# Kernel tuning notes

Hardware: AMD Instinct MI355X
Metric: run time of the kernel (lower is better)

Reference implementation:

```python
import jax, jax.numpy as jnp
import numpy as np

B, NB, D, H = 16384, 3, 1024, 8
HD = D // H
EPS = 1e-5

def setup_inputs() -> dict:
    key = jax.random.key(0)
    ks = jax.random.split(key, 24)
    w = lambda k, shp: jax.random.normal(k, shp, jnp.float32) * 0.02
    return {
        "x": jax.random.normal(ks[0], (B, NB, D), jnp.float32),
        # nn.MultiheadAttention params
        "in_proj_w": w(ks[1], (3 * D, D)),
        "in_proj_b": jnp.zeros((3 * D,), jnp.float32),
        "out_w": w(ks[2], (D, D)),
        "out_b": jnp.zeros((D,), jnp.float32),
        # weight_generator MLP
        "wg1_w": w(ks[3], (D, D * NB)), "wg1_b": jnp.zeros((D,), jnp.float32),
        "wg2_w": w(ks[4], (D // 2, D)), "wg2_b": jnp.zeros((D // 2,), jnp.float32),
        "wg3_w": w(ks[5], (NB, D // 2)), "wg3_b": jnp.zeros((NB,), jnp.float32),
        # refiner MLP + LayerNorms
        "r1_w": w(ks[6], (2 * D, D)), "r1_b": jnp.zeros((2 * D,), jnp.float32),
        "ln1_g": jnp.ones((2 * D,), jnp.float32), "ln1_b": jnp.zeros((2 * D,), jnp.float32),
        "r2_w": w(ks[7], (D, 2 * D)), "r2_b": jnp.zeros((D,), jnp.float32),
        "ln2_g": jnp.ones((D,), jnp.float32), "ln2_b": jnp.zeros((D,), jnp.float32),
    }

def _layernorm(x, g, b):
    m = jnp.mean(x, axis=-1, keepdims=True)
    v = jnp.mean(jnp.square(x - m), axis=-1, keepdims=True)
    return (x - m) * jax.lax.rsqrt(v + EPS) * g + b

def _forward(x, in_proj_w, in_proj_b, out_w, out_b,
             wg1_w, wg1_b, wg2_w, wg2_b, wg3_w, wg3_b,
             r1_w, r1_b, ln1_g, ln1_b, r2_w, r2_b, ln2_g, ln2_b):
    b = x.shape[0]
    # --- cross (self) attention over the NB branch tokens ---
    qkv = jnp.einsum("bsd,ed->bse", x, in_proj_w) + in_proj_b  # [B, NB, 3D]
    q, k, v = jnp.split(qkv, 3, axis=-1)
    q = q.reshape(b, NB, H, HD)
    k = k.reshape(b, NB, H, HD)
    v = v.reshape(b, NB, H, HD)
    scores = jnp.einsum("bqhd,bkhd->bhqk", q, k) / jnp.sqrt(jnp.float32(HD))
    attn = jax.nn.softmax(scores, axis=-1)
    o = jnp.einsum("bhqk,bkhd->bqhd", attn, v).reshape(b, NB, D)
    attended = jnp.einsum("bsd,ed->bse", o, out_w) + out_b  # [B, NB, D]
    # --- dynamic softmax gate over branches ---
    flat = attended.reshape(b, NB * D)
    h = jax.nn.relu(flat @ wg1_w.T + wg1_b)
    h = jax.nn.relu(h @ wg2_w.T + wg2_b)
    weights = jax.nn.softmax(h @ wg3_w.T + wg3_b, axis=-1)  # [B, NB]
    weighted = jnp.einsum("bsd,bs->bd", attended, weights)  # [B, D]
    # --- refiner (dropout inactive in eval) ---
    h = weighted @ r1_w.T + r1_b
    h = jax.nn.relu(_layernorm(h, ln1_g, ln1_b))
    out = h @ r2_w.T + r2_b
    return _layernorm(out, ln2_g, ln2_b)

def reference(x, in_proj_w, in_proj_b, out_w, out_b,
              wg1_w, wg1_b, wg2_w, wg2_b, wg3_w, wg3_b,
              r1_w, r1_b, ln1_g, ln1_b, r2_w, r2_b, ln2_g, ln2_b):
    return _forward(x, in_proj_w, in_proj_b, out_w, out_b,
                    wg1_w, wg1_b, wg2_w, wg2_b, wg3_w, wg3_b,
                    r1_w, r1_b, ln1_g, ln1_b, r2_w, r2_b, ln2_g, ln2_b)
```

## Files before the change

### kernel.cpp

```cpp
#include <hip/hip_runtime.h>
#include <hip/hip_bf16.h>

#define BB   16384
#define NBR  3
#define DD   1024
#define HH   8
#define HDD  128

typedef __attribute__((ext_vector_type(8))) short short8;
typedef __attribute__((ext_vector_type(4))) float f32x4;

__device__ __forceinline__ float b2f(ushort u) {
    union { unsigned int i; float f; } x; x.i = ((unsigned int)u) << 16; return x.f;
}
__device__ __forceinline__ ushort f2b(float f) {
    union { __hip_bfloat16 h; ushort u; } x; x.h = __float2bfloat16(f); return x.u;
}

__global__ __launch_bounds__(256) void cvt_f32_bf16(const float* __restrict__ in,
                                                    ushort* __restrict__ out, long n) {
    long i = ((long)blockIdx.x * 256 + threadIdx.x) * 4;
    if (i + 4 > n) return;
    float4 v = *reinterpret_cast<const float4*>(in + i);
    unsigned int a = ((unsigned int)f2b(v.x)) | (((unsigned int)f2b(v.y)) << 16);
    unsigned int b = ((unsigned int)f2b(v.z)) | (((unsigned int)f2b(v.w)) << 16);
    uint2 p; p.x = a; p.y = b;
    *reinterpret_cast<uint2*>(out + i) = p;
}

__global__ __launch_bounds__(256) void transpose_cvt(const float* __restrict__ in,
                                                     ushort* __restrict__ out) {
    __shared__ float t[32][33];
    const int bx = blockIdx.x & 31, by = blockIdx.x >> 5;
    const int tx = threadIdx.x & 31, ty = threadIdx.x >> 5;
    #pragma unroll
    for (int i = 0; i < 4; i++)
        t[ty + i * 8][tx] = in[(size_t)(by * 32 + ty + i * 8) * 1024 + bx * 32 + tx];
    __syncthreads();
    #pragma unroll
    for (int i = 0; i < 4; i++)
        out[(size_t)(bx * 32 + ty + i * 8) * 1024 + by * 32 + tx] = f2b(t[tx][ty + i * 8]);
}

__global__ __launch_bounds__(256) void bias1_kernel(const float* __restrict__ wg1w,
                                                    const float* __restrict__ wg1b,
                                                    const float* __restrict__ outb,
                                                    float* __restrict__ b1p) {
    const int o = (blockIdx.x * 256 + threadIdx.x) >> 6;
    const int lane = threadIdx.x & 63;
    const float* wr = wg1w + (size_t)o * 3072;
    float s = 0.f;
    for (int e = lane; e < 1024; e += 64)
        s += outb[e] * (wr[e] + wr[e + 1024] + wr[e + 2048]);
    #pragma unroll
    for (int off = 32; off; off >>= 1) s += __shfl_xor(s, off, 64);
    if (lane == 0) b1p[o] = s + wg1b[o];
}

__global__ __launch_bounds__(256) void biasfold_kernel(const float* __restrict__ w,
                                                       const float* __restrict__ bin,
                                                       const float* __restrict__ badd,
                                                       float* __restrict__ outb, int K) {
    const int o = (blockIdx.x * 256 + threadIdx.x) >> 6;
    const int lane = threadIdx.x & 63;
    const float* wr = w + (size_t)o * K;
    float s = 0.f;
    for (int e = lane; e < K; e += 64) s += bin[e] * wr[e];
    #pragma unroll
    for (int off = 32; off; off >>= 1) s += __shfl_xor(s, off, 64);
    if (lane == 0) outb[o] = s + badd[o];
}

#define CPAD 258
template<int EPI>
__global__ __launch_bounds__(512, 2)
void gemm256(const ushort* __restrict__ A, const ushort* __restrict__ Bt,
             const float* __restrict__ bias, void* __restrict__ Cout,
             int M, int N, int K) {
    extern __shared__ ushort lds[];

    const int tid  = threadIdx.x;
    const int wid  = tid >> 6;
    const int lane = tid & 63;
    const int cpx  = gridDim.x >> 3;
    const int bid  = (blockIdx.x & 7) * cpx + (blockIdx.x >> 3);
    const int nbn  = N >> 8;
    const int bm   = bid / nbn;
    const int bn   = bid % nbn;
    const long m0  = (long)bm * 256;
    const long n0  = (long)bn * 256;
    const int NT   = K >> 6;

    const int srow = tid >> 3;
    const int kel  = (((tid & 7) ^ (srow & 7)) << 3);
    const int widEl = wid * 512;

    const ushort* gA[2][2];
    const ushort* gB[2][2];
    #pragma unroll
    for (int c = 0; c < 2; c++)
        #pragma unroll
        for (int j = 0; j < 2; j++) {
            gA[c][j] = A  + (size_t)(m0 + c * 128 + j * 64 + srow) * K + kel;
            gB[c][j] = Bt + (size_t)(n0 + c * 128 + j * 64 + srow) * K + kel;
        }

    const int wr = wid >> 2, wc = wid & 3;
    const int lm15 = lane & 15;
    int aoff[8];
    #pragma unroll
    for (int m = 0; m < 8; m++) aoff[m] = (wr * 128 + m * 16 + lm15) * 64;
    int boff[4];
    #pragma unroll
    for (int c = 0; c < 4; c++) boff[c] = (wc * 64 + c * 16 + lm15) * 64;
    const int kbr[2] = {
        (((0 << 6) | ((lane >> 4) << 4)) ^ ((lane & 7) << 4)) >> 1,
        (((1 << 6) | ((lane >> 4) << 4)) ^ ((lane & 7) << 4)) >> 1
    };

    f32x4 acc[8][4];
    #pragma unroll
    for (int m = 0; m < 8; m++)
        #pragma unroll
        for (int c = 0; c < 4; c++) { f32x4 z = {0.f, 0.f, 0.f, 0.f}; acc[m][c] = z; }

    short8 af[8], af2[8], bf[2], bf2[2];

#define STAGE(C, PB, TT) { \
    const ushort* _g0; const ushort* _g1; int _b; \
    if ((C) < 2) { _g0 = gA[(C)][0] + (TT) * 64; _g1 = gA[(C)][1] + (TT) * 64; \
                   _b = (PB) * 16384 + (C) * 8192 + widEl; } \
    else         { _g0 = gB[(C) - 2][0] + (TT) * 64; _g1 = gB[(C) - 2][1] + (TT) * 64; \
                   _b = 32768 + (PB) * 16384 + ((C) - 2) * 8192 + widEl; } \
    __builtin_amdgcn_global_load_lds((const __attribute__((address_space(1))) void*)_g0, \
        (__attribute__((address_space(3))) void*)&lds[_b], 16, 0, 0); \
    __builtin_amdgcn_global_load_lds((const __attribute__((address_space(1))) void*)_g1, \
        (__attribute__((address_space(3))) void*)&lds[_b + 4096], 16, 0, 0); }

#define READ_A(DST, P, KK) { \
    _Pragma("unroll") \
    for (int _m = 0; _m < 8; _m++) \
        DST[_m] = *(const short8*)&lds[(P) * 16384 + aoff[_m] + kbr[KK]]; }

#define READ_B2(DST, P, KK, C0) { \
    DST[0] = *(const short8*)&lds[32768 + (P) * 16384 + boff[(C0)] + kbr[KK]]; \
    DST[1] = *(const short8*)&lds[32768 + (P) * 16384 + boff[(C0) + 1] + kbr[KK]]; }

#define MFMA8x2(AF, BF, C0) { \
    _Pragma("unroll") \
    for (int _m = 0; _m < 8; _m++) { \
        acc[_m][(C0)]     = __builtin_amdgcn_mfma_f32_16x16x32_bf16(AF[_m], BF[0], acc[_m][(C0)], 0, 0, 0); \
        acc[_m][(C0) + 1] = __builtin_amdgcn_mfma_f32_16x16x32_bf16(AF[_m], BF[1], acc[_m][(C0) + 1], 0, 0, 0); } }

#define TILE_STEP(P, T, PRE) { \
     \
    if (PRE) STAGE(0, (P) ^ 1, (T) + 1); \
    if (PRE) { asm volatile("s_waitcnt vmcnt(2)" ::: "memory"); } \
    else     { asm volatile("s_waitcnt vmcnt(0)" ::: "memory"); } \
    __builtin_amdgcn_s_barrier(); \
    asm volatile("" ::: "memory"); \
    __builtin_amdgcn_sched_barrier(0); \
     \
    READ_A(af, P, 0); \
    READ_B2(bf, P, 0, 0); \
    __builtin_amdgcn_s_setprio(1); MFMA8x2(af, bf, 0); __builtin_amdgcn_s_setprio(0); \
    if (PRE) STAGE(1, (P) ^ 1, (T) + 1); \
    READ_B2(bf2, P, 0, 2); \
    __builtin_amdgcn_s_barrier(); \
     \
    __builtin_amdgcn_s_setprio(1); MFMA8x2(af, bf2, 2); __builtin_amdgcn_s_setprio(0); \
    if (PRE) STAGE(2, (P) ^ 1, (T) + 1); \
    READ_A(af2, P, 1); \
    READ_B2(bf, P, 1, 0); \
    __builtin_amdgcn_s_barrier(); \
     \
    __builtin_amdgcn_s_setprio(1); MFMA8x2(af2, bf, 0); __builtin_amdgcn_s_setprio(0); \
    if (PRE) STAGE(3, (P) ^ 1, (T) + 1); \
    READ_B2(bf2, P, 1, 2); \
    __builtin_amdgcn_s_barrier(); \
     \
    __builtin_amdgcn_s_setprio(1); MFMA8x2(af2, bf2, 2); __builtin_amdgcn_s_setprio(0); \
    __builtin_amdgcn_s_barrier(); }

    STAGE(0, 0, 0); STAGE(1, 0, 0); STAGE(2, 0, 0); STAGE(3, 0, 0);

    int t = 0;
    for (; t + 2 < NT; t += 2) {
        TILE_STEP(0, t, true);
        TILE_STEP(1, t + 1, true);
    }
    TILE_STEP(0, t, true);
    TILE_STEP(1, t + 1, false);

#undef TILE_STEP
#undef MFMA8x2
#undef READ_B2
#undef READ_A
#undef STAGE

    const int l16 = lane >> 4;
    #pragma unroll
    for (int c = 0; c < 4; c++) {
        const int colc = wc * 64 + c * 16 + lm15;
        const float bc = bias[n0 + colc];
        #pragma unroll
        for (int m = 0; m < 8; m++) {
            const int rowb = wr * 128 + m * 16 + l16 * 4;
            #pragma unroll
            for (int j = 0; j < 4; j++) {
                float v = acc[m][c][j] + bc;
                if (EPI == 1) v = v > 0.f ? v : 0.f;
                lds[(rowb + j) * CPAD + colc] = f2b(v);
            }
        }
    }
    __syncthreads();
    {
        const int r0 = tid >> 5;
        const int c0 = (tid & 31) * 8;
        #pragma unroll
        for (int it = 0; it < 16; it++) {
            const int row = it * 16 + r0;
            short8 val = *(const short8*)&lds[row * CPAD + c0];
            *reinterpret_cast<short8*>(&((ushort*)Cout)[(m0 + row) * (long)N + n0 + c0]) = val;
        }
    }
}

template<int EPI>
__global__ __launch_bounds__(256, 2)
void gemm_bt(const ushort* __restrict__ A, const ushort* __restrict__ Bt,
             const float* __restrict__ bias, void* __restrict__ Cout,
             int M, int N, int K, int lda, int ldb, int ldc, int sA, int sC) {
    __shared__ ushort As[128 * 64];
    __shared__ ushort Bs[128 * 64];
    const int tid  = threadIdx.x;
    const int wid  = tid >> 6;
    const int lane = tid & 63;
    const int cpx  = gridDim.x >> 3;
    const int bid  = (blockIdx.x & 7) * cpx + (blockIdx.x >> 3);
    const int nbn  = N >> 7;
    const int bm   = bid / nbn;
    const int bn   = bid % nbn;
    const long m0  = (long)bm * 128;
    const long n0  = (long)bn * 128;

    A += (size_t)blockIdx.y * sA;
    const long cOff = (long)blockIdx.y * sC;

    const int srow = tid >> 3;
    const int scol = (tid & 7) << 3;
    const ushort* gA = A  + (m0 + srow) * (long)lda + scol;
    const ushort* gB = Bt + (n0 + srow) * (long)ldb + scol;

    f32x4 acc[4][4];
    #pragma unroll
    for (int i = 0; i < 4; i++)
        #pragma unroll
        for (int j = 0; j < 4; j++) { f32x4 z = {0.f, 0.f, 0.f, 0.f}; acc[i][j] = z; }

    const int wr = wid >> 1, wc = wid & 1;
    const int kits = K >> 6;

    for (int kt = 0; kt < kits; ++kt) {
        const ushort* pA = gA + kt * 64;
        const ushort* pB = gB + kt * 64;
        #pragma unroll
        for (int i = 0; i < 4; i++) {
            __builtin_amdgcn_global_load_lds(
                (const __attribute__((address_space(1))) void*)(pA + (long)i * 32 * lda),
                (__attribute__((address_space(3))) void*)&As[(i * 32 + wid * 8) * 64],
                16, 0, 0);
        }
        #pragma unroll
        for (int i = 0; i < 4; i++) {
            __builtin_amdgcn_global_load_lds(
                (const __attribute__((address_space(1))) void*)(pB + (long)i * 32 * ldb),
                (__attribute__((address_space(3))) void*)&Bs[(i * 32 + wid * 8) * 64],
                16, 0, 0);
        }
        __syncthreads();
        #pragma unroll
        for (int kk = 0; kk < 2; kk++) {
            const int ko = kk * 32 + (lane >> 4) * 8;
            short8 af[4], bf[4];
            #pragma unroll
            for (int m = 0; m < 4; m++)
                af[m] = *(const short8*)&As[(wr * 64 + m * 16 + (lane & 15)) * 64 + ko];
            #pragma unroll
            for (int n = 0; n < 4; n++)
                bf[n] = *(const short8*)&Bs[(wc * 64 + n * 16 + (lane & 15)) * 64 + ko];
            #pragma unroll
            for (int m = 0; m < 4; m++)
                #pragma unroll
                for (int n = 0; n < 4; n++)
                    acc[m][n] = __builtin_amdgcn_mfma_f32_16x16x32_bf16(af[m], bf[n], acc[m][n], 0, 0, 0);
        }
        __syncthreads();
    }

    #pragma unroll
    for (int n = 0; n < 4; n++) {
        const long c = n0 + wc * 64 + n * 16 + (lane & 15);
        const float bc = bias[c];
        #pragma unroll
        for (int m = 0; m < 4; m++) {
            const long r = m0 + wr * 64 + m * 16 + (lane >> 4) * 4;
            #pragma unroll
            for (int j = 0; j < 4; j++) {
                float v = acc[m][n][j] + bc;
                if (EPI == 1) v = v > 0.f ? v : 0.f;
                ((ushort*)Cout)[(r + j) * (long)ldc + cOff + c] = f2b(v);
            }
        }
    }
}

__global__ __launch_bounds__(256) void attn_kernel(const ushort* __restrict__ qkv,
                                                   ushort* __restrict__ o) {
    const int w    = (blockIdx.x * 256 + threadIdx.x) >> 6;
    const int lane = threadIdx.x & 63;
    const int b = w >> 3, h = w & 7;
    const ushort* base = qkv + (size_t)b * (3 * 3072) + h * HDD + lane * 2;

    float q[3][2], k[3][2], v[3][2];
    #pragma unroll
    for (int i = 0; i < 3; i++) {
        unsigned int qu = *(const unsigned int*)(base + i * 3072);
        unsigned int ku = *(const unsigned int*)(base + i * 3072 + 1024);
        unsigned int vu = *(const unsigned int*)(base + i * 3072 + 2048);
        q[i][0] = b2f((ushort)(qu & 0xffff)); q[i][1] = b2f((ushort)(qu >> 16));
        k[i][0] = b2f((ushort)(ku & 0xffff)); k[i][1] = b2f((ushort)(ku >> 16));
        v[i][0] = b2f((ushort)(vu & 0xffff)); v[i][1] = b2f((ushort)(vu >> 16));
    }

    float s[3][3];
    #pragma unroll
    for (int i = 0; i < 3; i++)
        #pragma unroll
        for (int j = 0; j < 3; j++)
            s[i][j] = q[i][0] * k[j][0] + q[i][1] * k[j][1];

    #pragma unroll
    for (int off = 32; off; off >>= 1)
        #pragma unroll
        for (int i = 0; i < 3; i++)
            #pragma unroll
            for (int j = 0; j < 3; j++)
                s[i][j] += __shfl_xor(s[i][j], off, 64);

    const float sc = 0.08838834764831845f;
    float a[3][3];
    #pragma unroll
    for (int i = 0; i < 3; i++) {
        float l0 = s[i][0] * sc, l1 = s[i][1] * sc, l2 = s[i][2] * sc;
        float mx = fmaxf(fmaxf(l0, l1), l2);
        float e0 = __expf(l0 - mx), e1 = __expf(l1 - mx), e2 = __expf(l2 - mx);
        float inv = 1.f / (e0 + e1 + e2);
        a[i][0] = e0 * inv; a[i][1] = e1 * inv; a[i][2] = e2 * inv;
    }

    ushort* ob = o + (size_t)b * 3072 + h * HDD + lane * 2;
    #pragma unroll
    for (int i = 0; i < 3; i++) {
        float o0 = a[i][0] * v[0][0] + a[i][1] * v[1][0] + a[i][2] * v[2][0];
        float o1 = a[i][0] * v[0][1] + a[i][1] * v[1][1] + a[i][2] * v[2][1];
        unsigned int pk = ((unsigned int)f2b(o0)) | (((unsigned int)f2b(o1)) << 16);
        *(unsigned int*)(ob + i * 1024) = pk;
    }
}

__global__ __launch_bounds__(256) void gate_kernel(const ushort* __restrict__ h2,
                                                   const float* __restrict__ w3,
                                                   const float* __restrict__ b3,
                                                   const ushort* __restrict__ att,
                                                   ushort* __restrict__ weighted) {
    const int gw = (blockIdx.x * 256 + threadIdx.x) >> 6;
    const int lane = threadIdx.x & 63;
    if (gw >= BB) return;

    const ushort* hr = h2 + (size_t)gw * 512 + lane * 8;
    short8 hv = *(const short8*)hr;
    float hf[8];
    #pragma unroll
    for (int d = 0; d < 8; d++) hf[d] = b2f((ushort)hv[d]);

    float dot[3];
    #pragma unroll
    for (int s = 0; s < 3; s++) {
        const float* wr = w3 + s * 512 + lane * 8;
        float4 wa = *(const float4*)wr;
        float4 wb = *(const float4*)(wr + 4);
        dot[s] = hf[0] * wa.x + hf[1] * wa.y + hf[2] * wa.z + hf[3] * wa.w
               + hf[4] * wb.x + hf[5] * wb.y + hf[6] * wb.z + hf[7] * wb.w;
    }
    #pragma unroll
    for (int off = 32; off; off >>= 1)
        #pragma unroll
        for (int s = 0; s < 3; s++) dot[s] += __shfl_xor(dot[s], off, 64);

    float l0 = dot[0] + b3[0], l1 = dot[1] + b3[1], l2 = dot[2] + b3[2];
    float mx = fmaxf(fmaxf(l0, l1), l2);
    float e0 = __expf(l0 - mx), e1 = __expf(l1 - mx), e2 = __expf(l2 - mx);
    float inv = 1.f / (e0 + e1 + e2);
    float w0 = e0 * inv, w1 = e1 * inv, w2 = e2 * inv;

    const ushort* ab = att + (size_t)gw * 3072;
    ushort* wb = weighted + (size_t)gw * 1024;
    #pragma unroll
    for (int i = 0; i < 2; i++) {
        int d0 = (i * 64 + lane) * 8;
        short8 a0 = *(const short8*)(ab + d0);
        short8 a1 = *(const short8*)(ab + 1024 + d0);
        short8 a2 = *(const short8*)(ab + 2048 + d0);
        short8 r;
        #pragma unroll
        for (int d = 0; d < 8; d++) {
            float v = w0 * b2f((ushort)a0[d]) + w1 * b2f((ushort)a1[d]) + w2 * b2f((ushort)a2[d]);
            r[d] = (short)f2b(v);
        }
        *(short8*)(wb + d0) = r;
    }
}

template<int W, int RELU, int OUTBF16>
__global__ __launch_bounds__(256) void ln_kernel(const ushort* __restrict__ in,
                                                 const float* __restrict__ g,
                                                 const float* __restrict__ bt,
                                                 void* __restrict__ out) {
    constexpr int E = W / 256;
    const int row = blockIdx.x;
    const ushort* xr = in + (size_t)row * W + threadIdx.x * E;

    float v[E];
    if (E == 8) {
        uint4 raw = *reinterpret_cast<const uint4*>(xr);
        const unsigned int* rw = (const unsigned int*)&raw;
        #pragma unroll
        for (int p = 0; p < 4; p++) {
            v[2 * p]     = b2f((ushort)(rw[p] & 0xffff));
            v[2 * p + 1] = b2f((ushort)(rw[p] >> 16));
        }
    } else {
        uint2 raw = *reinterpret_cast<const uint2*>(xr);
        const unsigned int* rw = (const unsigned int*)&raw;
        #pragma unroll
        for (int p = 0; p < 2; p++) {
            v[2 * p]     = b2f((ushort)(rw[p] & 0xffff));
            v[2 * p + 1] = b2f((ushort)(rw[p] >> 16));
        }
    }

    float s = 0.f;
    #pragma unroll
    for (int e = 0; e < E; e++) s += v[e];

    __shared__ float red1[4], red2[4];
    const int wid = threadIdx.x >> 6, lane = threadIdx.x & 63;
    #pragma unroll
    for (int off = 32; off; off >>= 1) s += __shfl_xor(s, off, 64);
    if (lane == 0) red1[wid] = s;
    __syncthreads();
    const float mean = (red1[0] + red1[1] + red1[2] + red1[3]) / (float)W;

    float q = 0.f;
    #pragma unroll
    for (int e = 0; e < E; e++) { float d = v[e] - mean; q += d * d; }
    #pragma unroll
    for (int off = 32; off; off >>= 1) q += __shfl_xor(q, off, 64);
    if (lane == 0) red2[wid] = q;
    __syncthreads();
    const float var = (red2[0] + red2[1] + red2[2] + red2[3]) / (float)W;
    const float rstd = rsqrtf(var + 1e-5f);

    const int c0 = threadIdx.x * E;
    float o[E];
    #pragma unroll
    for (int e = 0; e < E; e++) {
        float ov = (v[e] - mean) * rstd * g[c0 + e] + bt[c0 + e];
        if (RELU) ov = ov > 0.f ? ov : 0.f;
        o[e] = ov;
    }
    if (OUTBF16) {
        ushort* op = (ushort*)out + (size_t)row * W + c0;
        unsigned int pk[E / 2];
        #pragma unroll
        for (int p = 0; p < E / 2; p++)
            pk[p] = ((unsigned int)f2b(o[2 * p])) | (((unsigned int)f2b(o[2 * p + 1])) << 16);
        if (E == 8) *reinterpret_cast<uint4*>(op) = *(uint4*)pk;
        else        *reinterpret_cast<uint2*>(op) = *(uint2*)pk;
    } else {
        float* op = (float*)out + (size_t)row * W + c0;
        #pragma unroll
        for (int p = 0; p < E / 4; p++)
            reinterpret_cast<float4*>(op)[p] = ((float4*)o)[p];
    }
}

extern "C" void kernel_launch(void* const* d_in, const int* in_sizes, int n_in,
                              void* d_out, int out_size, void* d_ws, size_t ws_size,
                              hipStream_t stream) {
    const float* x    = (const float*)d_in[0];
    const float* ipw  = (const float*)d_in[1];
    const float* ipb  = (const float*)d_in[2];
    const float* outw = (const float*)d_in[3];
    const float* outb = (const float*)d_in[4];
    const float* wg1w = (const float*)d_in[5];
    const float* wg1b = (const float*)d_in[6];
    const float* wg2w = (const float*)d_in[7];
    const float* wg2b = (const float*)d_in[8];
    const float* wg3w = (const float*)d_in[9];
    const float* wg3b = (const float*)d_in[10];
    const float* r1w  = (const float*)d_in[11];
    const float* r1b  = (const float*)d_in[12];
    const float* ln1g = (const float*)d_in[13];
    const float* ln1b = (const float*)d_in[14];
    const float* r2w  = (const float*)d_in[15];
    const float* r2b  = (const float*)d_in[16];
    const float* ln2g = (const float*)d_in[17];
    const float* ln2b = (const float*)d_in[18];

    char* ws = (char*)d_ws;
    ushort* w_ip  = (ushort*)(ws + 0);
    ushort* w_g1  = (ushort*)(ws + 8388608);
    ushort* w_g2  = (ushort*)(ws + 14680064);
    ushort* w_r1  = (ushort*)(ws + 15728640);
    ushort* w_r2  = (ushort*)(ws + 19922944);
    char* R1 = ws + 24117248;
    char* R2 = ws + 124780544;

    ushort* xb       = (ushort*)R1;
    ushort* qkv      = (ushort*)R2;
    ushort* o_att    = (ushort*)R1;
    ushort* h1       = (ushort*)(R2 + 0);
    ushort* h2       = (ushort*)(R2 + 33554432);
    ushort* wsum_o   = (ushort*)(R2 + 50331648);
    ushort* r1out    = (ushort*)(R2 + 117440512);
    ushort* r2out    = (ushort*)(R2 + 184549376);
    ushort* w1p      = (ushort*)(R2 + 218103808);
    ushort* w_outT   = (ushort*)(R2 + 224395264);
    float*  b1p      = (float*) (R2 + 226492416);
    float*  zbias    = (float*) (R2 + 226496512);
    ushort* w_r1c    = (ushort*)(R2 + 226500608);
    float*  b_r1c    = (float*) (R2 + 230694912);
    ushort* ln1out   = (ushort*)R1;

    const int ldsBytes = 256 * CPAD * 2;
    (void)hipFuncSetAttribute((const void*)gemm256<0>, hipFuncAttributeMaxDynamicSharedMemorySize, ldsBytes);
    (void)hipFuncSetAttribute((const void*)gemm256<1>, hipFuncAttributeMaxDynamicSharedMemorySize, ldsBytes);

    cvt_f32_bf16<<<49152, 256, 0, stream>>>(x,    xb,   (long)49152 * 1024);
    cvt_f32_bf16<<<3072,  256, 0, stream>>>(ipw,  w_ip, (long)3072 * 1024);
    cvt_f32_bf16<<<3072,  256, 0, stream>>>(wg1w, w_g1, (long)1024 * 3072);
    cvt_f32_bf16<<<512,   256, 0, stream>>>(wg2w, w_g2, (long)512 * 1024);
    cvt_f32_bf16<<<2048,  256, 0, stream>>>(r1w,  w_r1, (long)2048 * 1024);
    cvt_f32_bf16<<<2048,  256, 0, stream>>>(r2w,  w_r2, (long)1024 * 2048);

    gemm256<0><<<192 * 12, 512, ldsBytes, stream>>>(xb, w_ip, ipb, qkv, 49152, 3072, 1024);
    attn_kernel<<<32768, 256, 0, stream>>>(qkv, o_att);

    (void)hipMemsetAsync(zbias, 0, 4096, stream);
    transpose_cvt<<<1024, 256, 0, stream>>>(outw, w_outT);
    gemm_bt<0><<<dim3(64, 3), 256, 0, stream>>>(w_g1, w_outT, zbias, w1p,
                                                1024, 1024, 1024, 3072, 1024, 3072, 1024, 1024);
    bias1_kernel<<<256, 256, 0, stream>>>(wg1w, wg1b, outb, b1p);
    gemm_bt<0><<<dim3(128, 1), 256, 0, stream>>>(w_r1, w_outT, zbias, w_r1c,
                                                 2048, 1024, 1024, 1024, 1024, 1024, 0, 0);
    biasfold_kernel<<<512, 256, 0, stream>>>(r1w, outb, r1b, b_r1c, 1024);

    gemm256<1><<<64 * 4, 512, ldsBytes, stream>>>(o_att, w1p, b1p, h1, 16384, 1024, 3072);
    gemm_bt<1><<<dim3(128 * 4, 1), 256, 0, stream>>>(h1, w_g2, wg2b, h2,
                                                     16384, 512, 1024, 1024, 1024, 512, 0, 0);
    gate_kernel<<<4096, 256, 0, stream>>>(h2, wg3w, wg3b, o_att, wsum_o);

    gemm256<0><<<64 * 8, 512, ldsBytes, stream>>>(wsum_o, w_r1c, b_r1c, r1out, 16384, 2048, 1024);
    ln_kernel<2048, 1, 1><<<16384, 256, 0, stream>>>(r1out, ln1g, ln1b, ln1out);
    gemm256<0><<<64 * 4, 512, ldsBytes, stream>>>(ln1out, w_r2, r2b, r2out, 16384, 1024, 2048);
    ln_kernel<1024, 0, 0><<<16384, 256, 0, stream>>>(r2out, ln2g, ln2b, d_out);
}
```

Baseline: 835.5 us.

## Make gemm256 persistent with next-tile prefetch overlapping the epilogue

Converts the 256x256 GEMM into a persistent kernel with 256 workgroups, each looping over several output tiles. The first k-slab of the next tile is prefetched into LDS while the current tile's epilogue runs, and the epilogue is split into two half-passes through a swizzled region of LDS. It also merges the five weight-conversion launches and the zero-bias memset into one kernel, and moves the small bias buffers into the weight region of the workspace. This removes per-block launch and prologue cost and hides the next tile's load latency, at the price of more synchronisation in the epilogue and a fixed tile-to-XCD mapping that requires the tile count to divide evenly.

Result: slower. 870.8 us (+4.2%).

```diff
diff --git a/kernel.cpp b/kernel.cpp
--- a/kernel.cpp
+++ b/kernel.cpp
@@ -26,6 +26,35 @@
     unsigned int b = ((unsigned int)f2b(v.z)) | (((unsigned int)f2b(v.w)) << 16);
     uint2 p; p.x = a; p.y = b;
     *reinterpret_cast<uint2*>(out + i) = p;
+}
+
+__global__ __launch_bounds__(256) void cvt_weights(const float* __restrict__ ipw,
+                                                   const float* __restrict__ wg1w,
+                                                   const float* __restrict__ wg2w,
+                                                   const float* __restrict__ r1w,
+                                                   const float* __restrict__ r2w,
+                                                   ushort* __restrict__ w_ip,
+                                                   ushort* __restrict__ w_g1,
+                                                   ushort* __restrict__ w_g2,
+                                                   ushort* __restrict__ w_r1,
+                                                   ushort* __restrict__ w_r2,
+                                                   float* __restrict__ zbias) {
+    if (blockIdx.x == 0) {
+        float4 z = {0.f, 0.f, 0.f, 0.f};
+        ((float4*)zbias)[threadIdx.x] = z;
+    }
+    long idx = (long)blockIdx.x * 256 + threadIdx.x;
+    const float* src; ushort* dst;
+    if (idx < 786432)                    { src = ipw;  dst = w_ip; }
+    else if ((idx -= 786432) < 786432)   { src = wg1w; dst = w_g1; }
+    else if ((idx -= 786432) < 131072)   { src = wg2w; dst = w_g2; }
+    else if ((idx -= 131072) < 524288)   { src = r1w;  dst = w_r1; }
+    else { idx -= 524288; if (idx >= 524288) return; src = r2w; dst = w_r2; }
+    float4 v = ((const float4*)src)[idx];
+    uint2 p;
+    p.x = ((unsigned int)f2b(v.x)) | (((unsigned int)f2b(v.y)) << 16);
+    p.y = ((unsigned int)f2b(v.z)) | (((unsigned int)f2b(v.w)) << 16);
+    ((uint2*)dst)[idx] = p;
 }
 
 __global__ __launch_bounds__(256) void transpose_cvt(const float* __restrict__ in,
@@ -71,39 +100,25 @@
     if (lane == 0) outb[o] = s + badd[o];
 }
 
-#define CPAD 258
 template<int EPI>
 __global__ __launch_bounds__(512, 2)
 void gemm256(const ushort* __restrict__ A, const ushort* __restrict__ Bt,
              const float* __restrict__ bias, void* __restrict__ Cout,
-             int M, int N, int K) {
+             int M, int N, int K, int ntiles) {
     extern __shared__ ushort lds[];
 
     const int tid  = threadIdx.x;
     const int wid  = tid >> 6;
     const int lane = tid & 63;
-    const int cpx  = gridDim.x >> 3;
-    const int bid  = (blockIdx.x & 7) * cpx + (blockIdx.x >> 3);
     const int nbn  = N >> 8;
-    const int bm   = bid / nbn;
-    const int bn   = bid % nbn;
-    const long m0  = (long)bm * 256;
-    const long n0  = (long)bn * 256;
-    const int NT   = K >> 6;
+    const int tpx  = ntiles >> 3;
+    const int G    = ntiles >> 8;
+    const int xcd  = blockIdx.x & 7;
+    const int kq   = blockIdx.x >> 3;
 
     const int srow = tid >> 3;
     const int kel  = (((tid & 7) ^ (srow & 7)) << 3);
     const int widEl = wid * 512;
-
-    const ushort* gA[2][2];
-    const ushort* gB[2][2];
-    #pragma unroll
-    for (int c = 0; c < 2; c++)
-        #pragma unroll
-        for (int j = 0; j < 2; j++) {
-            gA[c][j] = A  + (size_t)(m0 + c * 128 + j * 64 + srow) * K + kel;
-            gB[c][j] = Bt + (size_t)(n0 + c * 128 + j * 64 + srow) * K + kel;
-        }
 
     const int wr = wid >> 2, wc = wid & 3;
     const int lm15 = lane & 15;
@@ -117,12 +132,8 @@
         (((0 << 6) | ((lane >> 4) << 4)) ^ ((lane & 7) << 4)) >> 1,
         (((1 << 6) | ((lane >> 4) << 4)) ^ ((lane & 7) << 4)) >> 1
     };
-
-    f32x4 acc[8][4];
-    #pragma unroll
-    for (int m = 0; m < 8; m++)
-        #pragma unroll
-        for (int c = 0; c < 4; c++) { f32x4 z = {0.f, 0.f, 0.f, 0.f}; acc[m][c] = z; }
+    const int l16 = lane >> 4;
+    const int NT = K >> 6;
 
     short8 af[8], af2[8], bf[2], bf2[2];
 
@@ -153,78 +164,132 @@
         acc[_m][(C0) + 1] = __builtin_amdgcn_mfma_f32_16x16x32_bf16(AF[_m], BF[1], acc[_m][(C0) + 1], 0, 0, 0); } }
 
 #define TILE_STEP(P, T, PRE) { \
-     \
     if (PRE) STAGE(0, (P) ^ 1, (T) + 1); \
     if (PRE) { asm volatile("s_waitcnt vmcnt(2)" ::: "memory"); } \
     else     { asm volatile("s_waitcnt vmcnt(0)" ::: "memory"); } \
     __builtin_amdgcn_s_barrier(); \
     asm volatile("" ::: "memory"); \
     __builtin_amdgcn_sched_barrier(0); \
-     \
     READ_A(af, P, 0); \
     READ_B2(bf, P, 0, 0); \
     __builtin_amdgcn_s_setprio(1); MFMA8x2(af, bf, 0); __builtin_amdgcn_s_setprio(0); \
     if (PRE) STAGE(1, (P) ^ 1, (T) + 1); \
     READ_B2(bf2, P, 0, 2); \
     __builtin_amdgcn_s_barrier(); \
-     \
     __builtin_amdgcn_s_setprio(1); MFMA8x2(af, bf2, 2); __builtin_amdgcn_s_setprio(0); \
     if (PRE) STAGE(2, (P) ^ 1, (T) + 1); \
     READ_A(af2, P, 1); \
     READ_B2(bf, P, 1, 0); \
     __builtin_amdgcn_s_barrier(); \
-     \
     __builtin_amdgcn_s_setprio(1); MFMA8x2(af2, bf, 0); __builtin_amdgcn_s_setprio(0); \
     if (PRE) STAGE(3, (P) ^ 1, (T) + 1); \
     READ_B2(bf2, P, 1, 2); \
     __builtin_amdgcn_s_barrier(); \
-     \
     __builtin_amdgcn_s_setprio(1); MFMA8x2(af2, bf2, 2); __builtin_amdgcn_s_setprio(0); \
     __builtin_amdgcn_s_barrier(); }
 
-    STAGE(0, 0, 0); STAGE(1, 0, 0); STAGE(2, 0, 0); STAGE(3, 0, 0);
-
-    int t = 0;
-    for (; t + 2 < NT; t += 2) {
+    for (int g = 0; g < G; ++g) {
+        const int bid = xcd * tpx + g * 32 + kq;
+        const int bm  = bid / nbn;
+        const int bn  = bid % nbn;
+        const long m0 = (long)bm * 256;
+        const long n0 = (long)bn * 256;
+
+        const ushort* gA[2][2];
+        const ushort* gB[2][2];
+        #pragma unroll
+        for (int c = 0; c < 2; c++)
+            #pragma unroll
+            for (int j = 0; j < 2; j++) {
+                gA[c][j] = A  + (size_t)(m0 + c * 128 + j * 64 + srow) * K + kel;
+                gB[c][j] = Bt + (size_t)(n0 + c * 128 + j * 64 + srow) * K + kel;
+            }
+
+        f32x4 acc[8][4];
+        #pragma unroll
+        for (int m = 0; m < 8; m++)
+            #pragma unroll
+            for (int c = 0; c < 4; c++) { f32x4 z = {0.f, 0.f, 0.f, 0.f}; acc[m][c] = z; }
+
+        if (g == 0) {
+            STAGE(0, 0, 0); STAGE(1, 0, 0); STAGE(2, 0, 0); STAGE(3, 0, 0);
+        }
+
+        int t = 0;
+        for (; t + 2 < NT; t += 2) {
+            TILE_STEP(0, t, true);
+            TILE_STEP(1, t + 1, true);
+        }
         TILE_STEP(0, t, true);
-        TILE_STEP(1, t + 1, true);
-    }
-    TILE_STEP(0, t, true);
-    TILE_STEP(1, t + 1, false);
+        TILE_STEP(1, t + 1, false);
+
+        if (g + 1 < G) {
+            const int bid2 = xcd * tpx + (g + 1) * 32 + kq;
+            const int bm2  = bid2 / nbn;
+            const int bn2  = bid2 % nbn;
+            const long m02 = (long)bm2 * 256;
+            const long n02 = (long)bn2 * 256;
+            #pragma unroll
+            for (int c = 0; c < 2; c++)
+                #pragma unroll
+                for (int j = 0; j < 2; j++) {
+                    const ushort* a2 = A  + (size_t)(m02 + c * 128 + j * 64 + srow) * K + kel;
+                    const ushort* b2 = Bt + (size_t)(n02 + c * 128 + j * 64 + srow) * K + kel;
+                    __builtin_amdgcn_global_load_lds(
+                        (const __attribute__((address_space(1))) void*)a2,
+                        (__attribute__((address_space(3))) void*)&lds[c * 8192 + j * 4096 + widEl],
+                        16, 0, 0);
+                    __builtin_amdgcn_global_load_lds(
+                        (const __attribute__((address_space(1))) void*)b2,
+                        (__attribute__((address_space(3))) void*)&lds[32768 + c * 8192 + j * 4096 + widEl],
+                        16, 0, 0);
+                }
+        }
+
+        #pragma unroll
+        for (int s = 0; s < 2; ++s) {
+            const int cbase = wr ? 49152 : 16384;
+            #pragma unroll
+            for (int c = 0; c < 4; c++) {
+                const int colc = wc * 64 + c * 16 + lm15;
+                const float bc = bias[n0 + colc];
+                #pragma unroll
+                for (int mm = 0; mm < 4; mm++) {
+                    const int m = s * 4 + mm;
+                    #pragma unroll
+                    for (int j = 0; j < 4; j++) {
+                        const int srw = mm * 16 + l16 * 4 + j;
+                        float v = acc[m][c][j] + bc;
+                        if (EPI == 1) v = v > 0.f ? v : 0.f;
+                        const int scol = colc ^ (((srw >> 2) & 3) << 4);
+                        lds[cbase + srw * 256 + scol] = f2b(v);
+                    }
+                }
+            }
+            __syncthreads();
+            {
+                const int r0 = tid >> 5;
+                const int c0 = (tid & 31) * 8;
+                #pragma unroll
+                for (int it = 0; it < 8; it++) {
+                    const int slot = it * 16 + r0;
+                    const int srw  = slot & 63;
+                    const int base = (slot < 64) ? 16384 : 49152;
+                    const int scol = c0 ^ (((srw >> 2) & 3) << 4);
+                    short8 val = *(const short8*)&lds[base + srw * 256 + scol];
+                    const long grow = m0 + 64 * s + slot + ((slot >> 6) << 6);
+                    *reinterpret_cast<short8*>(&((ushort*)Cout)[grow * (long)N + n0 + c0]) = val;
+                }
+            }
+            __syncthreads();
+        }
+    }
 
 #undef TILE_STEP
 #undef MFMA8x2
 #undef READ_B2
 #undef READ_A
 #undef STAGE
-
-    const int l16 = lane >> 4;
-    #pragma unroll
-    for (int c = 0; c < 4; c++) {
-        const int colc = wc * 64 + c * 16 + lm15;
-        const float bc = bias[n0 + colc];
-        #pragma unroll
-        for (int m = 0; m < 8; m++) {
-            const int rowb = wr * 128 + m * 16 + l16 * 4;
-            #pragma unroll
-            for (int j = 0; j < 4; j++) {
-                float v = acc[m][c][j] + bc;
-                if (EPI == 1) v = v > 0.f ? v : 0.f;
-                lds[(rowb + j) * CPAD + colc] = f2b(v);
-            }
-        }
-    }
-    __syncthreads();
-    {
-        const int r0 = tid >> 5;
-        const int c0 = (tid & 31) * 8;
-        #pragma unroll
-        for (int it = 0; it < 16; it++) {
-            const int row = it * 16 + r0;
-            short8 val = *(const short8*)&lds[row * CPAD + c0];
-            *reinterpret_cast<short8*>(&((ushort*)Cout)[(m0 + row) * (long)N + n0 + c0]) = val;
-        }
-    }
 }
 
 template<int EPI>
@@ -522,6 +587,9 @@
 
     char* ws = (char*)d_ws;
     ushort* w_ip  = (ushort*)(ws + 0);
+    float*  zbias = (float*) (ws + 6291456);
+    float*  b1p   = (float*) (ws + 6295552);
+    float*  b_r1c = (float*) (ws + 6299648);
     ushort* w_g1  = (ushort*)(ws + 8388608);
     ushort* w_g2  = (ushort*)(ws + 14680064);
     ushort* w_r1  = (ushort*)(ws + 15728640);
@@ -539,27 +607,20 @@
     ushort* r2out    = (ushort*)(R2 + 184549376);
     ushort* w1p      = (ushort*)(R2 + 218103808);
     ushort* w_outT   = (ushort*)(R2 + 224395264);
-    float*  b1p      = (float*) (R2 + 226492416);
-    float*  zbias    = (float*) (R2 + 226496512);
     ushort* w_r1c    = (ushort*)(R2 + 226500608);
-    float*  b_r1c    = (float*) (R2 + 230694912);
     ushort* ln1out   = (ushort*)R1;
 
-    const int ldsBytes = 256 * CPAD * 2;
+    const int ldsBytes = 131072;
     (void)hipFuncSetAttribute((const void*)gemm256<0>, hipFuncAttributeMaxDynamicSharedMemorySize, ldsBytes);
     (void)hipFuncSetAttribute((const void*)gemm256<1>, hipFuncAttributeMaxDynamicSharedMemorySize, ldsBytes);
 
-    cvt_f32_bf16<<<49152, 256, 0, stream>>>(x,    xb,   (long)49152 * 1024);
-    cvt_f32_bf16<<<3072,  256, 0, stream>>>(ipw,  w_ip, (long)3072 * 1024);
-    cvt_f32_bf16<<<3072,  256, 0, stream>>>(wg1w, w_g1, (long)1024 * 3072);
-    cvt_f32_bf16<<<512,   256, 0, stream>>>(wg2w, w_g2, (long)512 * 1024);
-    cvt_f32_bf16<<<2048,  256, 0, stream>>>(r1w,  w_r1, (long)2048 * 1024);
-    cvt_f32_bf16<<<2048,  256, 0, stream>>>(r2w,  w_r2, (long)1024 * 2048);
-
-    gemm256<0><<<192 * 12, 512, ldsBytes, stream>>>(xb, w_ip, ipb, qkv, 49152, 3072, 1024);
+    cvt_f32_bf16<<<49152, 256, 0, stream>>>(x, xb, (long)49152 * 1024);
+    cvt_weights<<<10752, 256, 0, stream>>>(ipw, wg1w, wg2w, r1w, r2w,
+                                           w_ip, w_g1, w_g2, w_r1, w_r2, zbias);
+
+    gemm256<0><<<256, 512, ldsBytes, stream>>>(xb, w_ip, ipb, qkv, 49152, 3072, 1024, 2304);
     attn_kernel<<<32768, 256, 0, stream>>>(qkv, o_att);
 
-    (void)hipMemsetAsync(zbias, 0, 4096, stream);
     transpose_cvt<<<1024, 256, 0, stream>>>(outw, w_outT);
     gemm_bt<0><<<dim3(64, 3), 256, 0, stream>>>(w_g1, w_outT, zbias, w1p,
                                                 1024, 1024, 1024, 3072, 1024, 3072, 1024, 1024);
@@ -568,13 +629,13 @@
                                                  2048, 1024, 1024, 1024, 1024, 1024, 0, 0);
     biasfold_kernel<<<512, 256, 0, stream>>>(r1w, outb, r1b, b_r1c, 1024);
 
-    gemm256<1><<<64 * 4, 512, ldsBytes, stream>>>(o_att, w1p, b1p, h1, 16384, 1024, 3072);
+    gemm256<1><<<256, 512, ldsBytes, stream>>>(o_att, w1p, b1p, h1, 16384, 1024, 3072, 256);
     gemm_bt<1><<<dim3(128 * 4, 1), 256, 0, stream>>>(h1, w_g2, wg2b, h2,
                                                      16384, 512, 1024, 1024, 1024, 512, 0, 0);
     gate_kernel<<<4096, 256, 0, stream>>>(h2, wg3w, wg3b, o_att, wsum_o);
 
-    gemm256<0><<<64 * 8, 512, ldsBytes, stream>>>(wsum_o, w_r1c, b_r1c, r1out, 16384, 2048, 1024);
+    gemm256<0><<<256, 512, ldsBytes, stream>>>(wsum_o, w_r1c, b_r1c, r1out, 16384, 2048, 1024, 512);
     ln_kernel<2048, 1, 1><<<16384, 256, 0, stream>>>(r1out, ln1g, ln1b, ln1out);
-    gemm256<0><<<64 * 4, 512, ldsBytes, stream>>>(ln1out, w_r2, r2b, r2out, 16384, 1024, 2048);
+    gemm256<0><<<256, 512, ldsBytes, stream>>>(ln1out, w_r2, r2b, r2out, 16384, 1024, 2048, 256);
     ln_kernel<1024, 0, 0><<<16384, 256, 0, stream>>>(r2out, ln2g, ln2b, d_out);
 }
```
